# Optimization experiments

Hardware: AMD Instinct MI355X
Metric: run time of the kernel (lower is better)

The kernel has to match this reference:

```python
import jax, jax.numpy as jnp
import numpy as np

N = 50000
E = 800000
F_IN, F_HID, F_OUT = 128, 256, 128


def setup_inputs() -> dict:
    key = jax.random.key(0)
    ks = jax.random.split(key, 8)
    x = jax.random.normal(ks[0], (N, F_IN), dtype=jnp.float32)
    edge_index = jax.random.randint(ks[1], (2, E), 0, N, dtype=jnp.int64)
    # SAGEConv params: lin_l acts on aggregated neighbors (has bias), lin_r on root.
    def w(k, fi, fo):
        return jax.random.normal(k, (fi, fo), dtype=jnp.float32) / np.sqrt(fi)
    return {
        "x": x,
        "edge_index": edge_index,
        "W1_l": w(ks[2], F_IN, F_HID),
        "W1_r": w(ks[3], F_IN, F_HID),
        "b1": jnp.zeros((F_HID,), dtype=jnp.float32),
        "W2_l": w(ks[4], F_HID, F_OUT),
        "W2_r": w(ks[5], F_HID, F_OUT),
        "b2": jnp.zeros((F_OUT,), dtype=jnp.float32),
    }


def _sage_conv(x, src, dst, W_l, W_r, b):
    # mean aggregation of source features onto destination nodes
    msg_sum = jax.ops.segment_sum(x[src], dst, num_segments=N)   # [N, F]
    deg = jax.ops.segment_sum(jnp.ones((src.shape[0],), x.dtype), dst,
                              num_segments=N)                    # [N]
    mean = msg_sum / jnp.maximum(deg, 1.0)[:, None]
    return mean @ W_l + x @ W_r + b


def reference(x, edge_index, W1_l, W1_r, b1, W2_l, W2_r, b2):
    src, dst = edge_index[0], edge_index[1]
    h = jax.nn.relu(_sage_conv(x, src, dst, W1_l, W1_r, b1))
    # dropout is identity in eval mode (p=0.0)
    out = _sage_conv(h, src, dst, W2_l, W2_r, b2)
    return out
```

## Files before the change

### kernel.cpp

```cpp
#include <hip/hip_runtime.h>

constexpr int NN = 50000;
constexpr int EE = 800000;
constexpr int FI = 128;
constexpr int FO = 128;

typedef __attribute__((ext_vector_type(4))) float f32x4;
typedef __attribute__((ext_vector_type(8))) short bf16x8;

__device__ inline unsigned short f2bf(float f) {
    union { float f; unsigned u; } v; v.f = f;
    unsigned r = v.u + 0x7FFFu + ((v.u >> 16) & 1u);
    return (unsigned short)(r >> 16);
}
__device__ inline float bf2f(unsigned short u) {
    union { unsigned u; float f; } v; v.u = ((unsigned)u) << 16; return v.f;
}


__global__ void deg_i_kernel(const int* __restrict__ ei, int* __restrict__ cnt) {
    int e = blockIdx.x * blockDim.x + threadIdx.x;
    if (e < EE) atomicAdd(&cnt[ei[EE + e] << 4], 1);
}

constexpr int SCAN_NBLK = (NN + 1023) / 1024;

__global__ __launch_bounds__(1024) void scan_phase1(const int* __restrict__ cnt,
                                                    int* __restrict__ rowptr,
                                                    int* __restrict__ bsum,
                                                    float* __restrict__ rdeg) {
    __shared__ int wsum[16];
    const int tid = threadIdx.x;
    const int lane = tid & 63;
    const int wid = tid >> 6;
    int i = blockIdx.x * 1024 + tid;
    int v = (i < NN) ? cnt[i << 4] : 0;
    if (i < NN) rdeg[i] = 1.0f / fmaxf((float)v, 1.0f);
    int s = v;
#pragma unroll
    for (int off = 1; off < 64; off <<= 1) {
        int t = __shfl_up(s, off, 64);
        if (lane >= off) s += t;
    }
    if (lane == 63) wsum[wid] = s;
    __syncthreads();
    if (wid == 0) {
        int ws = (lane < 16) ? wsum[lane] : 0;
#pragma unroll
        for (int off = 1; off < 16; off <<= 1) {
            int t = __shfl_up(ws, off, 64);
            if (lane >= off) ws += t;
        }
        if (lane < 16) wsum[lane] = ws;
    }
    __syncthreads();
    int woff = (wid > 0) ? wsum[wid - 1] : 0;
    if (i < NN) rowptr[i] = woff + s - v;
    if (tid == 0) bsum[blockIdx.x] = wsum[15];
}

__global__ void scan_phase2(int* __restrict__ bsum) {
    int lane = threadIdx.x;
    int v = (lane < SCAN_NBLK) ? bsum[lane] : 0;
    int s = v;
#pragma unroll
    for (int off = 1; off < 64; off <<= 1) {
        int t = __shfl_up(s, off, 64);
        if (lane >= off) s += t;
    }
    if (lane < SCAN_NBLK) bsum[lane] = s - v;
}

__global__ void scan_phase3(int* __restrict__ rowptr, const int* __restrict__ bsum) {
    int i = blockIdx.x * blockDim.x + threadIdx.x;
    if (i < NN) rowptr[i] += bsum[i >> 10];
    else if (i == NN) rowptr[NN] = EE;
}

__global__ void slot_kernel(const int* __restrict__ ei,
                            const int* __restrict__ rowptr,
                            int* __restrict__ cnt,
                            int* __restrict__ csr_src) {
    int e = blockIdx.x * blockDim.x + threadIdx.x;
    if (e < EE) {
        int src = ei[e];
        int dst = ei[EE + e];
        int old = atomicSub(&cnt[dst << 4], 1);
        csr_src[rowptr[dst] + old - 1] = src;
    }
}


__global__ __launch_bounds__(256) void gather_mean_bf16(
    const int* __restrict__ rowptr, const int* __restrict__ csr_src,
    const float* __restrict__ rdeg,
    unsigned short* __restrict__ A1)
{
    int node = blockIdx.x * 4 + (threadIdx.x >> 6);
    if (node >= NN) return;
    int lane = threadIdx.x & 63;
    int f = lane * 2;
    int start = rowptr[node];
    int end = rowptr[node + 1];
    float ax[8], ay[8];
#pragma unroll
    for (int u = 0; u < 8; ++u) { ax[u] = 0.f; ay[u] = 0.f; }
    for (int j = start; j < end; j += 8) {
        int si[8];
        float w[8];
#pragma unroll
        for (int u = 0; u < 8; ++u) {
            int idx = j + u;
            si[u] = csr_src[idx < end ? idx : start];
            w[u] = (idx < end) ? 1.f : 0.f;
        }
        ushort2 v[8];
#pragma unroll
        for (int u = 0; u < 8; ++u)
            v[u] = *reinterpret_cast<const ushort2*>(A1 + (size_t)si[u] * 256 + 128 + f);
#pragma unroll
        for (int u = 0; u < 8; ++u) {
            ax[u] = fmaf(w[u], bf2f(v[u].x), ax[u]);
            ay[u] = fmaf(w[u], bf2f(v[u].y), ay[u]);
        }
    }
    float s = rdeg[node];
    float sx = ((ax[0] + ax[1]) + (ax[2] + ax[3])) + ((ax[4] + ax[5]) + (ax[6] + ax[7]));
    float sy = ((ay[0] + ay[1]) + (ay[2] + ay[3])) + ((ay[4] + ay[5]) + (ay[6] + ay[7]));
    ushort2 o;
    o.x = f2bf(sx * s);
    o.y = f2bf(sy * s);
    *reinterpret_cast<ushort2*>(A1 + (size_t)node * 256 + f) = o;
}

__global__ __launch_bounds__(256) void gather_accum_f32(
    const int* __restrict__ rowptr, const int* __restrict__ csr_src,
    const float* __restrict__ rdeg, const unsigned short* __restrict__ g2b,
    float* __restrict__ outp)
{
    int node = blockIdx.x * 4 + (threadIdx.x >> 6);
    if (node >= NN) return;
    int lane = threadIdx.x & 63;
    int f = lane * 2;
    int start = rowptr[node];
    int end = rowptr[node + 1];
    float ax[8], ay[8];
#pragma unroll
    for (int u = 0; u < 8; ++u) { ax[u] = 0.f; ay[u] = 0.f; }
    for (int j = start; j < end; j += 8) {
        int si[8];
        float w[8];
#pragma unroll
        for (int u = 0; u < 8; ++u) {
            int idx = j + u;
            si[u] = csr_src[idx < end ? idx : start];
            w[u] = (idx < end) ? 1.f : 0.f;
        }
        ushort2 v[8];
#pragma unroll
        for (int u = 0; u < 8; ++u)
            v[u] = *reinterpret_cast<const ushort2*>(g2b + (size_t)si[u] * 128 + f);
#pragma unroll
        for (int u = 0; u < 8; ++u) {
            ax[u] = fmaf(w[u], bf2f(v[u].x), ax[u]);
            ay[u] = fmaf(w[u], bf2f(v[u].y), ay[u]);
        }
    }
    float s = rdeg[node];
    float sx = ((ax[0] + ax[1]) + (ax[2] + ax[3])) + ((ax[4] + ax[5]) + (ax[6] + ax[7]));
    float sy = ((ay[0] + ay[1]) + (ay[2] + ay[3])) + ((ay[4] + ay[5]) + (ay[6] + ay[7]));
    float* p = outp + (size_t)node * FO + f;
    float2 o = *reinterpret_cast<float2*>(p);
    o.x += sx * s;
    o.y += sy * s;
    *reinterpret_cast<float2*>(p) = o;
}


__global__ void cast_x_kernel(const float* __restrict__ x,
                              unsigned short* __restrict__ A1) {
    int i = blockIdx.x * blockDim.x + threadIdx.x;
    if (i >= NN * 32) return;
    int n = i >> 5;
    int c4 = (i & 31) * 4;
    float4 v = *reinterpret_cast<const float4*>(x + (size_t)n * FI + c4);
    ushort4 o;
    o.x = f2bf(v.x); o.y = f2bf(v.y); o.z = f2bf(v.z); o.w = f2bf(v.w);
    *reinterpret_cast<ushort4*>(A1 + (size_t)n * 256 + 128 + c4) = o;
}

__global__ void prep_weights(const float* __restrict__ W1l, const float* __restrict__ W1r,
                             const float* __restrict__ W2l, const float* __restrict__ W2r,
                             unsigned short* __restrict__ B1T,
                             unsigned short* __restrict__ B2T) {
    int i = blockIdx.x * blockDim.x + threadIdx.x;
    if (i >= 256 * 256) return;
    int n = i >> 8, k = i & 255;
    float v1 = (k < 128) ? W1l[(size_t)k * 256 + n] : W1r[(size_t)(k - 128) * 256 + n];
    B1T[(size_t)n * 256 + k] = f2bf(v1);
    float v2 = (n < 128) ? W2r[(size_t)k * 128 + n] : W2l[(size_t)k * 128 + (n - 128)];
    B2T[(size_t)n * 256 + k] = f2bf(v2);
}

constexpr int GPAD = 72;

template<int MODE>
__global__ __launch_bounds__(256) void mfma_gemm(
    const unsigned short* __restrict__ A,
    const unsigned short* __restrict__ BT,
    const float* __restrict__ bias,
    unsigned short* __restrict__ out_bf,
    float* __restrict__ out_f0,
    unsigned short* __restrict__ g2b)
{
    __shared__ unsigned short Al[64][GPAD];
    __shared__ unsigned short Bl[256][GPAD];

    const int t = threadIdx.x;
    const int wid = t >> 6;
    const int wr = wid >> 1;
    const int wc = wid & 1;
    const int lane = t & 63;
    const int l15 = lane & 15;
    const int lhi = lane >> 4;
    const int row0 = blockIdx.x * 64;

    f32x4 acc[2][8];
#pragma unroll
    for (int m = 0; m < 2; ++m)
#pragma unroll
        for (int n = 0; n < 8; ++n) acc[m][n] = f32x4{0.f, 0.f, 0.f, 0.f};

    for (int kc = 0; kc < 256; kc += 64) {
        __syncthreads();
#pragma unroll
        for (int i = 0; i < 2; ++i) {
            int idx = t + i * 256;
            int r = idx >> 3;
            int c = (idx & 7) * 8;
            int rr = row0 + r;
            if (rr >= NN) rr = NN - 1;
            *reinterpret_cast<uint4*>(&Al[r][c]) =
                *reinterpret_cast<const uint4*>(A + (size_t)rr * 256 + kc + c);
        }
#pragma unroll
        for (int i = 0; i < 8; ++i) {
            int idx = t + i * 256;
            int r = idx >> 3;
            int c = (idx & 7) * 8;
            *reinterpret_cast<uint4*>(&Bl[r][c]) =
                *reinterpret_cast<const uint4*>(BT + (size_t)r * 256 + kc + c);
        }
        __syncthreads();
#pragma unroll
        for (int ks = 0; ks < 64; ks += 32) {
            bf16x8 a0 = *reinterpret_cast<const bf16x8*>(&Al[wr * 32 + l15][ks + lhi * 8]);
            bf16x8 a1 = *reinterpret_cast<const bf16x8*>(&Al[wr * 32 + 16 + l15][ks + lhi * 8]);
#pragma unroll
            for (int n = 0; n < 8; ++n) {
                bf16x8 b = *reinterpret_cast<const bf16x8*>(
                    &Bl[wc * 128 + n * 16 + l15][ks + lhi * 8]);
                acc[0][n] = __builtin_amdgcn_mfma_f32_16x16x32_bf16(a0, b, acc[0][n], 0, 0, 0);
                acc[1][n] = __builtin_amdgcn_mfma_f32_16x16x32_bf16(a1, b, acc[1][n], 0, 0, 0);
            }
        }
    }

#pragma unroll
    for (int n = 0; n < 8; ++n) {
        int col = wc * 128 + n * 16 + l15;
#pragma unroll
        for (int m = 0; m < 2; ++m) {
#pragma unroll
            for (int j = 0; j < 4; ++j) {
                int row = row0 + wr * 32 + m * 16 + lhi * 4 + j;
                if (row < NN) {
                    float v = acc[m][n][j];
                    if (MODE == 0) {
                        v += bias[col];
                        v = fmaxf(v, 0.f);
                        out_bf[(size_t)row * 256 + col] = f2bf(v);
                    } else {
                        if (col < 128) out_f0[(size_t)row * 128 + col] = v + bias[col];
                        else           g2b[(size_t)row * 128 + (col - 128)] = f2bf(v);
                    }
                }
            }
        }
    }
}


extern "C" void kernel_launch(void* const* d_in, const int* in_sizes, int n_in,
                              void* d_out, int out_size, void* d_ws, size_t ws_size,
                              hipStream_t stream) {
    const float* x   = (const float*)d_in[0];
    const int*   ei  = (const int*)d_in[1];
    const float* W1l = (const float*)d_in[2];
    const float* W1r = (const float*)d_in[3];
    const float* b1  = (const float*)d_in[4];
    const float* W2l = (const float*)d_in[5];
    const float* W2r = (const float*)d_in[6];
    const float* b2  = (const float*)d_in[7];
    float*       out = (float*)d_out;

    const size_t needed =
        ((size_t)NN * 16 + (NN + 16) + EE + NN
         + (size_t)NN * 128 * 2 + 65536 + 64) * 4;
    if (ws_size < needed) return;

    int*            cnt     = (int*)d_ws;
    int*            rowptr  = cnt + (size_t)NN * 16;
    int*            csr_src = rowptr + (NN + 16);
    float*          rdeg    = (float*)(csr_src + EE);
    unsigned short* A1      = (unsigned short*)(rdeg + NN);
    unsigned short* g2b     = A1;
    unsigned short* h       = A1 + (size_t)NN * 256;
    unsigned short* B1T     = h + (size_t)NN * 256;
    unsigned short* B2T     = B1T + 256 * 256;
    int*            bsum    = (int*)(B2T + 256 * 256);

    hipMemsetAsync(cnt, 0, (size_t)NN * 16 * sizeof(int), stream);
    prep_weights<<<256, 256, 0, stream>>>(W1l, W1r, W2l, W2r, B1T, B2T);
    cast_x_kernel<<<(NN * 32 + 255) / 256, 256, 0, stream>>>(x, A1);
    deg_i_kernel<<<(EE + 255) / 256, 256, 0, stream>>>(ei, cnt);
    scan_phase1<<<SCAN_NBLK, 1024, 0, stream>>>(cnt, rowptr, bsum, rdeg);
    scan_phase2<<<1, 64, 0, stream>>>(bsum);
    scan_phase3<<<(NN + 256) / 256, 256, 0, stream>>>(rowptr, bsum);
    slot_kernel<<<(EE + 255) / 256, 256, 0, stream>>>(ei, rowptr, cnt, csr_src);

    gather_mean_bf16<<<(NN + 3) / 4, 256, 0, stream>>>(rowptr, csr_src, rdeg, A1);
    mfma_gemm<0><<<(NN + 63) / 64, 256, 0, stream>>>(A1, B1T, b1, h, nullptr, nullptr);

    mfma_gemm<1><<<(NN + 63) / 64, 256, 0, stream>>>(h, B2T, b2, nullptr, out, g2b);

    gather_accum_f32<<<(NN + 3) / 4, 256, 0, stream>>>(rowptr, csr_src, rdeg, g2b, out);
}
```

Baseline: 328.3 us.

## Persistent GEMM with resident B half-tile and range-partitioned CSR slot fill

The GEMM becomes persistent. It uses 512 blocks, and each block loads one 128-column half of the transposed weight matrix into LDS once. It then loops over 128-row chunks, reading A fragments straight from global memory into registers, which removes repeated B staging and per-K-step syncs. The CSR slot kernel now has each block scan a chunk of edges but handle only destinations in one of eight node ranges. This is meant to localise atomic and scatter traffic. The trade-offs are that edge indices are read eight times, the persistent grid may underfill the device, and A loads are no longer coalesced through LDS.

Result: slower. 366.5 us (+11.6%).

```diff
diff --git a/kernel.cpp b/kernel.cpp
--- a/kernel.cpp
+++ b/kernel.cpp
@@ -77,16 +77,26 @@
     else if (i == NN) rowptr[NN] = EE;
 }
 
+constexpr int EDGE_CHUNK = 16384;
+constexpr int NCHUNKE = (EE + EDGE_CHUNK - 1) / EDGE_CHUNK;
+constexpr int DRANGE = NN / 8;
+
 __global__ void slot_kernel(const int* __restrict__ ei,
                             const int* __restrict__ rowptr,
                             int* __restrict__ cnt,
                             int* __restrict__ csr_src) {
-    int e = blockIdx.x * blockDim.x + threadIdx.x;
-    if (e < EE) {
-        int src = ei[e];
+    int rng = blockIdx.x & 7;
+    int chunk = blockIdx.x >> 3;
+    int lo = rng * DRANGE;
+    int hi = lo + DRANGE;
+    int e0 = chunk * EDGE_CHUNK;
+    int e1 = min(e0 + EDGE_CHUNK, EE);
+    for (int e = e0 + threadIdx.x; e < e1; e += 256) {
         int dst = ei[EE + e];
-        int old = atomicSub(&cnt[dst << 4], 1);
-        csr_src[rowptr[dst] + old - 1] = src;
+        if (dst >= lo && dst < hi) {
+            int old = atomicSub(&cnt[dst << 4], 1);
+            csr_src[rowptr[dst] + old - 1] = ei[e];
+        }
     }
 }
 
@@ -202,7 +212,9 @@
     B2T[(size_t)n * 256 + k] = f2bf(v2);
 }
 
-constexpr int GPAD = 72;
+constexpr int BPAD = 264;
+constexpr int NCHUNK = (NN + 127) / 128;
+constexpr int GEMM_BLK = 512;
 
 template<int MODE>
 __global__ __launch_bounds__(256) void mfma_gemm(
@@ -213,76 +225,74 @@
     float* __restrict__ out_f0,
     unsigned short* __restrict__ g2b)
 {
-    __shared__ unsigned short Al[64][GPAD];
-    __shared__ unsigned short Bl[256][GPAD];
+    __shared__ unsigned short Bl[128][BPAD];
 
     const int t = threadIdx.x;
     const int wid = t >> 6;
-    const int wr = wid >> 1;
-    const int wc = wid & 1;
     const int lane = t & 63;
     const int l15 = lane & 15;
     const int lhi = lane >> 4;
-    const int row0 = blockIdx.x * 64;
-
-    f32x4 acc[2][8];
-#pragma unroll
-    for (int m = 0; m < 2; ++m)
-#pragma unroll
-        for (int n = 0; n < 8; ++n) acc[m][n] = f32x4{0.f, 0.f, 0.f, 0.f};
-
-    for (int kc = 0; kc < 256; kc += 64) {
-        __syncthreads();
-#pragma unroll
-        for (int i = 0; i < 2; ++i) {
-            int idx = t + i * 256;
-            int r = idx >> 3;
-            int c = (idx & 7) * 8;
-            int rr = row0 + r;
-            if (rr >= NN) rr = NN - 1;
-            *reinterpret_cast<uint4*>(&Al[r][c]) =
-                *reinterpret_cast<const uint4*>(A + (size_t)rr * 256 + kc + c);
-        }
-#pragma unroll
-        for (int i = 0; i < 8; ++i) {
-            int idx = t + i * 256;
-            int r = idx >> 3;
-            int c = (idx & 7) * 8;
-            *reinterpret_cast<uint4*>(&Bl[r][c]) =
-                *reinterpret_cast<const uint4*>(BT + (size_t)r * 256 + kc + c);
-        }
-        __syncthreads();
-#pragma unroll
-        for (int ks = 0; ks < 64; ks += 32) {
-            bf16x8 a0 = *reinterpret_cast<const bf16x8*>(&Al[wr * 32 + l15][ks + lhi * 8]);
-            bf16x8 a1 = *reinterpret_cast<const bf16x8*>(&Al[wr * 32 + 16 + l15][ks + lhi * 8]);
+    const int half = blockIdx.x & 1;
+    const int bslot = blockIdx.x >> 1;
+
+    for (int i = t; i < 128 * 32; i += 256) {
+        int r = i >> 5;
+        int c = (i & 31) * 8;
+        *reinterpret_cast<uint4*>(&Bl[r][c]) =
+            *reinterpret_cast<const uint4*>(BT + ((size_t)(half * 128 + r)) * 256 + c);
+    }
+    __syncthreads();
+
+    for (int chunk = bslot; chunk < NCHUNK; chunk += GEMM_BLK / 2) {
+        const int rb = chunk * 128 + wid * 32;
+
+        bf16x8 a[2][8];
+#pragma unroll
+        for (int m = 0; m < 2; ++m) {
+            int row = rb + m * 16 + l15;
+            if (row >= NN) row = NN - 1;
+            const unsigned short* ap = A + (size_t)row * 256 + lhi * 8;
+#pragma unroll
+            for (int ks = 0; ks < 8; ++ks)
+                a[m][ks] = *reinterpret_cast<const bf16x8*>(ap + ks * 32);
+        }
+
+        f32x4 acc[2][8];
+#pragma unroll
+        for (int m = 0; m < 2; ++m)
+#pragma unroll
+            for (int n = 0; n < 8; ++n) acc[m][n] = f32x4{0.f, 0.f, 0.f, 0.f};
+
+#pragma unroll
+        for (int ks = 0; ks < 8; ++ks) {
 #pragma unroll
             for (int n = 0; n < 8; ++n) {
                 bf16x8 b = *reinterpret_cast<const bf16x8*>(
-                    &Bl[wc * 128 + n * 16 + l15][ks + lhi * 8]);
-                acc[0][n] = __builtin_amdgcn_mfma_f32_16x16x32_bf16(a0, b, acc[0][n], 0, 0, 0);
-                acc[1][n] = __builtin_amdgcn_mfma_f32_16x16x32_bf16(a1, b, acc[1][n], 0, 0, 0);
+                    &Bl[n * 16 + l15][ks * 32 + lhi * 8]);
+                acc[0][n] = __builtin_amdgcn_mfma_f32_16x16x32_bf16(a[0][ks], b, acc[0][n], 0, 0, 0);
+                acc[1][n] = __builtin_amdgcn_mfma_f32_16x16x32_bf16(a[1][ks], b, acc[1][n], 0, 0, 0);
             }
         }
-    }
-
-#pragma unroll
-    for (int n = 0; n < 8; ++n) {
-        int col = wc * 128 + n * 16 + l15;
-#pragma unroll
-        for (int m = 0; m < 2; ++m) {
-#pragma unroll
-            for (int j = 0; j < 4; ++j) {
-                int row = row0 + wr * 32 + m * 16 + lhi * 4 + j;
-                if (row < NN) {
-                    float v = acc[m][n][j];
-                    if (MODE == 0) {
-                        v += bias[col];
-                        v = fmaxf(v, 0.f);
-                        out_bf[(size_t)row * 256 + col] = f2bf(v);
-                    } else {
-                        if (col < 128) out_f0[(size_t)row * 128 + col] = v + bias[col];
-                        else           g2b[(size_t)row * 128 + (col - 128)] = f2bf(v);
+
+#pragma unroll
+        for (int n = 0; n < 8; ++n) {
+            int colh = n * 16 + l15;
+            int col = half * 128 + colh;
+#pragma unroll
+            for (int m = 0; m < 2; ++m) {
+#pragma unroll
+                for (int j = 0; j < 4; ++j) {
+                    int row = rb + m * 16 + lhi * 4 + j;
+                    if (row < NN) {
+                        float v = acc[m][n][j];
+                        if (MODE == 0) {
+                            v += bias[col];
+                            v = fmaxf(v, 0.f);
+                            out_bf[(size_t)row * 256 + col] = f2bf(v);
+                        } else {
+                            if (half == 0) out_f0[(size_t)row * 128 + colh] = v + bias[colh];
+                            else           g2b[(size_t)row * 128 + colh] = f2bf(v);
+                        }
                     }
                 }
             }
@@ -327,12 +337,12 @@
     scan_phase1<<<SCAN_NBLK, 1024, 0, stream>>>(cnt, rowptr, bsum, rdeg);
     scan_phase2<<<1, 64, 0, stream>>>(bsum);
     scan_phase3<<<(NN + 256) / 256, 256, 0, stream>>>(rowptr, bsum);
-    slot_kernel<<<(EE + 255) / 256, 256, 0, stream>>>(ei, rowptr, cnt, csr_src);
+    slot_kernel<<<NCHUNKE * 8, 256, 0, stream>>>(ei, rowptr, cnt, csr_src);
 
     gather_mean_bf16<<<(NN + 3) / 4, 256, 0, stream>>>(rowptr, csr_src, rdeg, A1);
-    mfma_gemm<0><<<(NN + 63) / 64, 256, 0, stream>>>(A1, B1T, b1, h, nullptr, nullptr);
-
-    mfma_gemm<1><<<(NN + 63) / 64, 256, 0, stream>>>(h, B2T, b2, nullptr, out, g2b);
+    mfma_gemm<0><<<GEMM_BLK, 256, 0, stream>>>(A1, B1T, b1, h, nullptr, nullptr);
+
+    mfma_gemm<1><<<GEMM_BLK, 256, 0, stream>>>(h, B2T, b2, nullptr, out, g2b);
 
     gather_accum_f32<<<(NN + 3) / 4, 256, 0, stream>>>(rowptr, csr_src, rdeg, g2b, out);
 }
```
